# Optimization experiments

Hardware: AMD Instinct MI355X
Metric: run time of the kernel (lower is better)

Reference implementation:

```python
import jax, jax.numpy as jnp
from jax import lax
import numpy as np

B = 8192      # device_size (world_size = 1 -> batch_size == device_size)
D = 512       # projection dim
K = 2048      # number of sampled negatives per anchor
TEMP = 0.5    # temperature
EPS = 1e-8    # torch CosineSimilarity eps


def setup_inputs() -> dict:
    key = jax.random.key(0)
    k1, k2, k3 = jax.random.split(key, 3)
    z_i = jax.random.normal(k1, (B, D), dtype=jnp.float32)
    z_j = jax.random.normal(k2, (B, D), dtype=jnp.float32)
    # neg_perm = torch.randperm(batch_size - 1)[:K]
    neg_perm = jax.random.permutation(k3, B - 1)[:K].astype(jnp.int32)
    return {"z_i": z_i, "z_j": z_j, "neg_perm": neg_perm}


def _logits(z_i, z_j, neg_perm):
    # cosine similarity matrix: (zi . zj) / max(||zi||*||zj||, eps), scaled by 1/T
    ni = jnp.linalg.norm(z_i, axis=1)                       # [B]
    nj = jnp.linalg.norm(z_j, axis=1)                       # [B]
    dots = jnp.einsum('id,jd->ij', z_i, z_j)                # [B,B]
    sim = dots / jnp.maximum(ni[:, None] * nj[None, :], EPS) / TEMP

    pos = jnp.diagonal(sim)                                 # [B] positives
    # row i of sim with diagonal removed has column k -> original column k + (k>=i)
    rows = jnp.arange(B, dtype=neg_perm.dtype)[:, None]     # [B,1]
    cols = neg_perm[None, :] + (neg_perm[None, :] >= rows).astype(neg_perm.dtype)  # [B,K]
    negs = jnp.take_along_axis(sim, cols, axis=1)           # [B,K]
    logits = jnp.concatenate([pos[:, None], negs], axis=1)  # [B,1+K], label = 0
    return logits, pos


def reference(z_i, z_j, neg_perm):
    logits, pos = _logits(z_i, z_j, neg_perm)
    # log(exp(pos) + sum exp(negs)) - pos == logsumexp(logits) - pos
    loss = jnp.sum(jax.nn.logsumexp(logits, axis=1) - pos) / B
    # top-1 / top-5 accuracy against label 0
    _, pred = lax.top_k(logits, 5)                          # [B,5]
    acc1 = jnp.mean((pred[:, 0] == 0).astype(jnp.float32)) * 100.0
    acc5 = jnp.mean(jnp.any(pred == 0, axis=1).astype(jnp.float32)) * 100.0
    return loss, acc1, acc5
```

## Files before the change

### kernel.cpp

```cpp
#include <hip/hip_runtime.h>
#include <cstdint>

#define B_SZ 8192
#define D_SZ 512
#define K_SZ 2048
#define EPSV 1e-8f
#define INV_T 2.0f

typedef float floatx16 __attribute__((ext_vector_type(16)));
typedef int intx8 __attribute__((ext_vector_type(8)));

__device__ __forceinline__ void async_cp16(const void* g, void* l) {
    typedef __attribute__((address_space(1))) unsigned int gds_t;
    typedef __attribute__((address_space(3))) unsigned int lds_t;
    __builtin_amdgcn_global_load_lds((gds_t*)(unsigned long long)g, (lds_t*)l, 16, 0, 0);
}

__device__ __forceinline__ int2 pack_fp8x8(float4 a0, float4 a1) {
    int w0 = __builtin_amdgcn_cvt_pk_fp8_f32(a0.x, a0.y, 0, false);
    w0 = __builtin_amdgcn_cvt_pk_fp8_f32(a0.z, a0.w, w0, true);
    int w1 = __builtin_amdgcn_cvt_pk_fp8_f32(a1.x, a1.y, 0, false);
    w1 = __builtin_amdgcn_cvt_pk_fp8_f32(a1.z, a1.w, w1, true);
    return make_int2(w0, w1);
}

__global__ __launch_bounds__(256) void k_prep(
    const float* __restrict__ zi, const float* __restrict__ zj,
    const int* __restrict__ perm,
    float* __restrict__ ri_arr, float* __restrict__ pos_arr,
    unsigned char* __restrict__ A,
    float4* __restrict__ kmeta, unsigned char* __restrict__ G,
    float* __restrict__ rowacc, float* __restrict__ out)
{
    int w = threadIdx.x >> 6, l = threadIdx.x & 63;
    if (blockIdx.x < 2048) {
        if (blockIdx.x < 64)
            rowacc[blockIdx.x * 256 + threadIdx.x] = 0.f;
        if (blockIdx.x == 0 && threadIdx.x < 3) out[threadIdx.x] = 0.f;
        int row = blockIdx.x * 4 + w;
        const float4* zi4 = (const float4*)(zi + (size_t)row * D_SZ);
        const float4* zj4 = (const float4*)(zj + (size_t)row * D_SZ);
        float4 a0 = zi4[2 * l], a1 = zi4[2 * l + 1];
        float4 b0 = zj4[2 * l], b1 = zj4[2 * l + 1];
        float si = a0.x * a0.x + a0.y * a0.y + a0.z * a0.z + a0.w * a0.w
                 + a1.x * a1.x + a1.y * a1.y + a1.z * a1.z + a1.w * a1.w;
        float sj = b0.x * b0.x + b0.y * b0.y + b0.z * b0.z + b0.w * b0.w
                 + b1.x * b1.x + b1.y * b1.y + b1.z * b1.z + b1.w * b1.w;
        float dd = a0.x * b0.x + a0.y * b0.y + a0.z * b0.z + a0.w * b0.w
                 + a1.x * b1.x + a1.y * b1.y + a1.z * b1.z + a1.w * b1.w;
        for (int m = 1; m < 64; m <<= 1) {
            si += __shfl_xor(si, m);
            sj += __shfl_xor(sj, m);
            dd += __shfl_xor(dd, m);
        }
        if (l == 0) {
            float ni = sqrtf(si), nj = sqrtf(sj);
            ri_arr[row] = INV_T / fmaxf(ni, 1e-6f);
            pos_arr[row] = dd / fmaxf(ni * nj, EPSV) * INV_T;
        }
        *(int2*)(A + (size_t)row * D_SZ + l * 8) = pack_fp8x8(a0, a1);
    } else {
        __shared__ float srj[4];
        int g = (blockIdx.x - 2048) * 4 + w;
        int c0 = perm[g >> 1];
        int c = c0 + (g & 1);
        const float4* src = (const float4*)(zj + (size_t)c * D_SZ);
        float4 a0 = src[2 * l], a1 = src[2 * l + 1];
        float s = a0.x * a0.x + a0.y * a0.y + a0.z * a0.z + a0.w * a0.w
                + a1.x * a1.x + a1.y * a1.y + a1.z * a1.z + a1.w * a1.w;
        for (int m = 1; m < 64; m <<= 1) s += __shfl_xor(s, m);
        if (l == 0) srj[w] = 1.0f / fmaxf(sqrtf(s), 1e-6f);
        __syncthreads();
        if ((w & 1) == 0 && l == 0)
            kmeta[g >> 1] = make_float4(srj[w], srj[w + 1],
                                        __int_as_float(c0), 0.f);
        *(int2*)(G + (size_t)g * D_SZ + l * 8) = pack_fp8x8(a0, a1);
    }
}

__global__ __launch_bounds__(256, 4) void k_gemm(
    const unsigned char* __restrict__ A,
    const unsigned char* __restrict__ G,
    const float4* __restrict__ kmeta,
    const float* __restrict__ ri_arr,
    const float* __restrict__ pos_arr,
    float* __restrict__ rowacc)
{
    __shared__ unsigned char Asl[2][128 * 64];
    __shared__ unsigned char Gsl[2][128 * 64];
    const int tid = threadIdx.x;
    const int l = tid & 63, w = tid >> 6;
    const int wm = w >> 1, wn = w & 1;
    const int ln = l & 31, q = l >> 5;

    const int bid = blockIdx.x;
    const int xcd = bid & 7;
    const int slot = bid >> 3;
    const int gTile = xcd * 4 + (slot & 3);
    const int aTile = slot >> 2;
    const int gBase = gTile * 128;
    const int aBase = aTile * 128;

    size_t aOff[2], gOff[2];
    int ldsOff[2];
    #pragma unroll
    for (int it = 0; it < 2; ++it) {
        int fc = it * 256 + tid;
        int r = fc >> 2, s = fc & 3;
        int scc = s ^ ((r ^ (r >> 2)) & 3);
        aOff[it] = (size_t)(aBase + r) * D_SZ + scc * 16;
        gOff[it] = (size_t)(gBase + r) * D_SZ + scc * 16;
        ldsOff[it] = fc * 16;
    }

    floatx16 acc[2][2] = {};

    int aAddr[2][2], gAddr[2][2];
    #pragma unroll
    for (int t = 0; t < 2; ++t) {
        int ar = wn * 64 + t * 32 + ln;
        int xa = (ar ^ (ar >> 2)) & 3;
        aAddr[t][0] = ar * 64 + ((2 * q) ^ xa) * 16;
        aAddr[t][1] = ar * 64 + ((2 * q + 1) ^ xa) * 16;
        int gr = wm * 64 + t * 32 + ln;
        int xg = (gr ^ (gr >> 2)) & 3;
        gAddr[t][0] = gr * 64 + ((2 * q) ^ xg) * 16;
        gAddr[t][1] = gr * 64 + ((2 * q + 1) ^ xg) * 16;
    }

    #pragma unroll
    for (int it = 0; it < 2; ++it) {
        async_cp16(A + aOff[it], &Asl[0][ldsOff[it]]);
        async_cp16(G + gOff[it], &Gsl[0][ldsOff[it]]);
    }

    #pragma unroll 1
    for (int dblk = 0; dblk < 8; ++dblk) {
        const int cur = dblk & 1, nxt = cur ^ 1;
        __syncthreads();
        if (dblk < 7) {
            #pragma unroll
            for (int it = 0; it < 2; ++it) {
                async_cp16(A + aOff[it] + (size_t)(dblk + 1) * 64, &Asl[nxt][ldsOff[it]]);
                async_cp16(G + gOff[it] + (size_t)(dblk + 1) * 64, &Gsl[nxt][ldsOff[it]]);
            }
        }
        intx8 af[2], gf[2];
        #pragma unroll
        for (int t = 0; t < 2; ++t) {
            int4 lo = *(const int4*)&Asl[cur][aAddr[t][0]];
            int4 hi = *(const int4*)&Asl[cur][aAddr[t][1]];
            af[t][0] = lo.x; af[t][1] = lo.y; af[t][2] = lo.z; af[t][3] = lo.w;
            af[t][4] = hi.x; af[t][5] = hi.y; af[t][6] = hi.z; af[t][7] = hi.w;
            int4 glo = *(const int4*)&Gsl[cur][gAddr[t][0]];
            int4 ghi = *(const int4*)&Gsl[cur][gAddr[t][1]];
            gf[t][0] = glo.x; gf[t][1] = glo.y; gf[t][2] = glo.z; gf[t][3] = glo.w;
            gf[t][4] = ghi.x; gf[t][5] = ghi.y; gf[t][6] = ghi.z; gf[t][7] = ghi.w;
        }
        #pragma unroll
        for (int tm = 0; tm < 2; ++tm)
            #pragma unroll
            for (int tn = 0; tn < 2; ++tn)
                acc[tm][tn] = __builtin_amdgcn_mfma_scale_f32_32x32x64_f8f6f4(
                    gf[tm], af[tn], acc[tm][tn],
                    0, 0,
                    0, 0x7f7f7f7f,
                    0, 0x7f7f7f7f);
    }

    int anc[2]; float riv[2], pv[2], pe[2] = {0.f, 0.f}, pc[2] = {0.f, 0.f};
    #pragma unroll
    for (int tn = 0; tn < 2; ++tn) {
        anc[tn] = aBase + wn * 64 + tn * 32 + ln;
        riv[tn] = ri_arr[anc[tn]];
        pv[tn] = pos_arr[anc[tn]];
    }
    #pragma unroll
    for (int tm = 0; tm < 2; ++tm) {
        #pragma unroll
        for (int j = 0; j < 4; ++j) {
            int k0 = gTile * 64 + wm * 32 + tm * 16 + 4 * j + 2 * q;
            float4 m0 = kmeta[k0];
            float4 m1 = kmeta[k0 + 1];
            #pragma unroll
            for (int p = 0; p < 2; ++p) {
                float4 md = p ? m1 : m0;
                int c0 = __float_as_int(md.z);
                int re = 4 * j + 2 * p;
                #pragma unroll
                for (int tn = 0; tn < 2; ++tn) {
                    bool sel = (c0 >= anc[tn]);
                    float v = sel ? acc[tm][tn][re + 1] : acc[tm][tn][re];
                    float rj = sel ? md.y : md.x;
                    float logit = v * riv[tn] * rj;
                    pe[tn] += __expf(logit);
                    pc[tn] += (logit > pv[tn]) ? 1.f : 0.f;
                }
            }
        }
    }
    #pragma unroll
    for (int tn = 0; tn < 2; ++tn) {
        pe[tn] += __shfl_xor(pe[tn], 32);
        pc[tn] += __shfl_xor(pc[tn], 32);
        if (q == 0) {
            atomicAdd(&rowacc[anc[tn]], pe[tn]);
            atomicAdd(&rowacc[B_SZ + anc[tn]], pc[tn]);
        }
    }
}

__global__ __launch_bounds__(256) void k_final(
    const float* __restrict__ rowacc, const float* __restrict__ pos_arr,
    float* __restrict__ out)
{
    int row = blockIdx.x * 256 + threadIdx.x;
    float pe = rowacc[row];
    float pc = rowacc[B_SZ + row];
    float pos = pos_arr[row];
    float loss = logf(__expf(pos) + pe) - pos;
    float a1 = (pc < 0.5f) ? 1.f : 0.f;
    float a5 = (pc < 4.5f) ? 1.f : 0.f;
    for (int m = 1; m < 64; m <<= 1) {
        loss += __shfl_xor(loss, m);
        a1 += __shfl_xor(a1, m);
        a5 += __shfl_xor(a5, m);
    }
    __shared__ float red[3][4];
    int w = threadIdx.x >> 6, l = threadIdx.x & 63;
    if (l == 0) { red[0][w] = loss; red[1][w] = a1; red[2][w] = a5; }
    __syncthreads();
    if (threadIdx.x == 0) {
        float L = red[0][0] + red[0][1] + red[0][2] + red[0][3];
        float A1 = red[1][0] + red[1][1] + red[1][2] + red[1][3];
        float A5 = red[2][0] + red[2][1] + red[2][2] + red[2][3];
        atomicAdd(&out[0], L / (float)B_SZ);
        atomicAdd(&out[1], A1 * (100.f / (float)B_SZ));
        atomicAdd(&out[2], A5 * (100.f / (float)B_SZ));
    }
}

extern "C" void kernel_launch(void* const* d_in, const int* in_sizes, int n_in,
                              void* d_out, int out_size, void* d_ws, size_t ws_size,
                              hipStream_t stream)
{
    const float* zi = (const float*)d_in[0];
    const float* zj = (const float*)d_in[1];
    const int* perm = (const int*)d_in[2];
    float* out = (float*)d_out;

    char* p = (char*)d_ws;
    unsigned char* A = (unsigned char*)p;    p += (size_t)B_SZ * D_SZ;
    unsigned char* G = (unsigned char*)p;    p += (size_t)2 * K_SZ * D_SZ;
    float* ri_arr = (float*)p;               p += (size_t)B_SZ * 4;
    float* pos_arr = (float*)p;              p += (size_t)B_SZ * 4;
    float4* kmeta = (float4*)p;              p += (size_t)K_SZ * 16;
    float* rowacc = (float*)p;               p += (size_t)2 * B_SZ * 4;

    k_prep<<<2048 + 1024, 256, 0, stream>>>(zi, zj, perm, ri_arr, pos_arr, A,
                                            kmeta, G, rowacc, out);
    k_gemm<<<2048, 256, 0, stream>>>(A, G, kmeta, ri_arr, pos_arr, rowacc);
    k_final<<<32, 256, 0, stream>>>(rowacc, pos_arr, out);
}
```

Measured before the change: 47.44 us.

## Enlarge GEMM tiles to 256x256 with 512 threads and 4-stage async pipeline

The FP8 MFMA GEMM moves from 128x128 tiles with 4 waves to 256x256 tiles with 8 waves per block, and launches 512 blocks instead of 2048. Global-to-LDS copies become a 4-deep ring buffer with explicit vmcnt waits and raw s_barrier, plus setprio around the MFMA cluster. The aim is more data reuse per loaded byte and better overlap of loads with compute. In exchange it uses 128KB of LDS per block, which lowers occupancy. It also relies on hand-counted vmcnt values being correct.

```diff
diff --git a/kernel.cpp b/kernel.cpp
--- a/kernel.cpp
+++ b/kernel.cpp
@@ -78,7 +78,7 @@
     }
 }
 
-__global__ __launch_bounds__(256, 4) void k_gemm(
+__global__ __launch_bounds__(512, 2) void k_gemm(
     const unsigned char* __restrict__ A,
     const unsigned char* __restrict__ G,
     const float4* __restrict__ kmeta,
@@ -86,8 +86,7 @@
     const float* __restrict__ pos_arr,
     float* __restrict__ rowacc)
 {
-    __shared__ unsigned char Asl[2][128 * 64];
-    __shared__ unsigned char Gsl[2][128 * 64];
+    __shared__ unsigned char lds[4][2][16384];
     const int tid = threadIdx.x;
     const int l = tid & 63, w = tid >> 6;
     const int wm = w >> 1, wn = w & 1;
@@ -96,16 +95,16 @@
     const int bid = blockIdx.x;
     const int xcd = bid & 7;
     const int slot = bid >> 3;
-    const int gTile = xcd * 4 + (slot & 3);
-    const int aTile = slot >> 2;
-    const int gBase = gTile * 128;
-    const int aBase = aTile * 128;
+    const int gTile = xcd * 2 + (slot & 1);
+    const int aTile = slot >> 1;
+    const int gBase = gTile * 256;
+    const int aBase = aTile * 256;
 
     size_t aOff[2], gOff[2];
     int ldsOff[2];
     #pragma unroll
     for (int it = 0; it < 2; ++it) {
-        int fc = it * 256 + tid;
+        int fc = it * 512 + tid;
         int r = fc >> 2, s = fc & 3;
         int scc = s ^ ((r ^ (r >> 2)) & 3);
         aOff[it] = (size_t)(aBase + r) * D_SZ + scc * 16;
@@ -113,65 +112,80 @@
         ldsOff[it] = fc * 16;
     }
 
-    floatx16 acc[2][2] = {};
-
-    int aAddr[2][2], gAddr[2][2];
-    #pragma unroll
-    for (int t = 0; t < 2; ++t) {
-        int ar = wn * 64 + t * 32 + ln;
+#define STAGE(t_) do {                                                      \
+        unsigned char* Ad_ = &lds[(t_) & 3][0][0];                          \
+        unsigned char* Gd_ = &lds[(t_) & 3][1][0];                          \
+        size_t ko_ = (size_t)(t_) * 64;                                     \
+        async_cp16(A + aOff[0] + ko_, Ad_ + ldsOff[0]);                     \
+        async_cp16(A + aOff[1] + ko_, Ad_ + ldsOff[1]);                     \
+        async_cp16(G + gOff[0] + ko_, Gd_ + ldsOff[0]);                     \
+        async_cp16(G + gOff[1] + ko_, Gd_ + ldsOff[1]);                     \
+    } while (0)
+
+    int aAddr[4][2], gAddr[2][2];
+    #pragma unroll
+    for (int tn = 0; tn < 4; ++tn) {
+        int ar = wn * 128 + tn * 32 + ln;
         int xa = (ar ^ (ar >> 2)) & 3;
-        aAddr[t][0] = ar * 64 + ((2 * q) ^ xa) * 16;
-        aAddr[t][1] = ar * 64 + ((2 * q + 1) ^ xa) * 16;
-        int gr = wm * 64 + t * 32 + ln;
+        aAddr[tn][0] = ar * 64 + ((2 * q) ^ xa) * 16;
+        aAddr[tn][1] = ar * 64 + ((2 * q + 1) ^ xa) * 16;
+    }
+    #pragma unroll
+    for (int tm = 0; tm < 2; ++tm) {
+        int gr = wm * 64 + tm * 32 + ln;
         int xg = (gr ^ (gr >> 2)) & 3;
-        gAddr[t][0] = gr * 64 + ((2 * q) ^ xg) * 16;
-        gAddr[t][1] = gr * 64 + ((2 * q + 1) ^ xg) * 16;
-    }
-
-    #pragma unroll
-    for (int it = 0; it < 2; ++it) {
-        async_cp16(A + aOff[it], &Asl[0][ldsOff[it]]);
-        async_cp16(G + gOff[it], &Gsl[0][ldsOff[it]]);
-    }
+        gAddr[tm][0] = gr * 64 + ((2 * q) ^ xg) * 16;
+        gAddr[tm][1] = gr * 64 + ((2 * q + 1) ^ xg) * 16;
+    }
+
+    floatx16 acc[2][4] = {};
+
+    STAGE(0); STAGE(1); STAGE(2);
 
     #pragma unroll 1
-    for (int dblk = 0; dblk < 8; ++dblk) {
-        const int cur = dblk & 1, nxt = cur ^ 1;
-        __syncthreads();
-        if (dblk < 7) {
-            #pragma unroll
-            for (int it = 0; it < 2; ++it) {
-                async_cp16(A + aOff[it] + (size_t)(dblk + 1) * 64, &Asl[nxt][ldsOff[it]]);
-                async_cp16(G + gOff[it] + (size_t)(dblk + 1) * 64, &Gsl[nxt][ldsOff[it]]);
-            }
-        }
-        intx8 af[2], gf[2];
-        #pragma unroll
-        for (int t = 0; t < 2; ++t) {
-            int4 lo = *(const int4*)&Asl[cur][aAddr[t][0]];
-            int4 hi = *(const int4*)&Asl[cur][aAddr[t][1]];
-            af[t][0] = lo.x; af[t][1] = lo.y; af[t][2] = lo.z; af[t][3] = lo.w;
-            af[t][4] = hi.x; af[t][5] = hi.y; af[t][6] = hi.z; af[t][7] = hi.w;
-            int4 glo = *(const int4*)&Gsl[cur][gAddr[t][0]];
-            int4 ghi = *(const int4*)&Gsl[cur][gAddr[t][1]];
-            gf[t][0] = glo.x; gf[t][1] = glo.y; gf[t][2] = glo.z; gf[t][3] = glo.w;
-            gf[t][4] = ghi.x; gf[t][5] = ghi.y; gf[t][6] = ghi.z; gf[t][7] = ghi.w;
-        }
+    for (int t = 0; t < 8; ++t) {
+        if (t < 6)       asm volatile("s_waitcnt vmcnt(8)" ::: "memory");
+        else if (t == 6) asm volatile("s_waitcnt vmcnt(4)" ::: "memory");
+        else             asm volatile("s_waitcnt vmcnt(0)" ::: "memory");
+        __builtin_amdgcn_s_barrier();
+        __builtin_amdgcn_sched_barrier(0);
+        if (t < 5) STAGE(t + 3);
+        const unsigned char* Ab = &lds[t & 3][0][0];
+        const unsigned char* Gb = &lds[t & 3][1][0];
+        intx8 af[4], gf[2];
+        #pragma unroll
+        for (int tn = 0; tn < 4; ++tn) {
+            int4 lo = *(const int4*)(Ab + aAddr[tn][0]);
+            int4 hi = *(const int4*)(Ab + aAddr[tn][1]);
+            af[tn][0] = lo.x; af[tn][1] = lo.y; af[tn][2] = lo.z; af[tn][3] = lo.w;
+            af[tn][4] = hi.x; af[tn][5] = hi.y; af[tn][6] = hi.z; af[tn][7] = hi.w;
+        }
+        #pragma unroll
+        for (int tm = 0; tm < 2; ++tm) {
+            int4 lo = *(const int4*)(Gb + gAddr[tm][0]);
+            int4 hi = *(const int4*)(Gb + gAddr[tm][1]);
+            gf[tm][0] = lo.x; gf[tm][1] = lo.y; gf[tm][2] = lo.z; gf[tm][3] = lo.w;
+            gf[tm][4] = hi.x; gf[tm][5] = hi.y; gf[tm][6] = hi.z; gf[tm][7] = hi.w;
+        }
+        __builtin_amdgcn_s_setprio(1);
         #pragma unroll
         for (int tm = 0; tm < 2; ++tm)
             #pragma unroll
-            for (int tn = 0; tn < 2; ++tn)
+            for (int tn = 0; tn < 4; ++tn)
                 acc[tm][tn] = __builtin_amdgcn_mfma_scale_f32_32x32x64_f8f6f4(
                     gf[tm], af[tn], acc[tm][tn],
                     0, 0,
                     0, 0x7f7f7f7f,
                     0, 0x7f7f7f7f);
-    }
-
-    int anc[2]; float riv[2], pv[2], pe[2] = {0.f, 0.f}, pc[2] = {0.f, 0.f};
-    #pragma unroll
-    for (int tn = 0; tn < 2; ++tn) {
-        anc[tn] = aBase + wn * 64 + tn * 32 + ln;
+        __builtin_amdgcn_s_setprio(0);
+    }
+#undef STAGE
+
+    int anc[4]; float riv[4], pv[4];
+    float pe[4] = {0.f, 0.f, 0.f, 0.f}, pc[4] = {0.f, 0.f, 0.f, 0.f};
+    #pragma unroll
+    for (int tn = 0; tn < 4; ++tn) {
+        anc[tn] = aBase + wn * 128 + tn * 32 + ln;
         riv[tn] = ri_arr[anc[tn]];
         pv[tn] = pos_arr[anc[tn]];
     }
@@ -179,7 +193,7 @@
     for (int tm = 0; tm < 2; ++tm) {
         #pragma unroll
         for (int j = 0; j < 4; ++j) {
-            int k0 = gTile * 64 + wm * 32 + tm * 16 + 4 * j + 2 * q;
+            int k0 = gTile * 128 + wm * 32 + tm * 16 + 4 * j + 2 * q;
             float4 m0 = kmeta[k0];
             float4 m1 = kmeta[k0 + 1];
             #pragma unroll
@@ -188,7 +202,7 @@
                 int c0 = __float_as_int(md.z);
                 int re = 4 * j + 2 * p;
                 #pragma unroll
-                for (int tn = 0; tn < 2; ++tn) {
+                for (int tn = 0; tn < 4; ++tn) {
                     bool sel = (c0 >= anc[tn]);
                     float v = sel ? acc[tm][tn][re + 1] : acc[tm][tn][re];
                     float rj = sel ? md.y : md.x;
@@ -200,7 +214,7 @@
         }
     }
     #pragma unroll
-    for (int tn = 0; tn < 2; ++tn) {
+    for (int tn = 0; tn < 4; ++tn) {
         pe[tn] += __shfl_xor(pe[tn], 32);
         pc[tn] += __shfl_xor(pc[tn], 32);
         if (q == 0) {
@@ -259,6 +273,6 @@
 
     k_prep<<<2048 + 1024, 256, 0, stream>>>(zi, zj, perm, ri_arr, pos_arr, A,
                                             kmeta, G, rowacc, out);
-    k_gemm<<<2048, 256, 0, stream>>>(A, G, kmeta, ri_arr, pos_arr, rowacc);
+    k_gemm<<<512, 512, 0, stream>>>(A, G, kmeta, ri_arr, pos_arr, rowacc);
     k_final<<<32, 256, 0, stream>>>(rowacc, pos_arr, out);
 }
```

Result: slower. 52.07 us (+9.8%).

## Sort negatives by column and split into shifted/unshifted halves to skip tiles

Applied to the files above, without the earlier changes.

The prep kernel now ranks each sampled negative by its column index, a counting sort done with a full pass over the permutation in every block. It writes the unshifted (c0) and shifted (c0+1) rows of z_j into two separate sorted halves of G, each with its own metadata. Each GEMM block handles one half and exits early when the tile's column range cannot contribute to its anchor rows (v=0 needs c0 < anchor, v=1 needs c0 >= anchor). This drops roughly half of the MFMA work in exchange for an O(K) rank computation per prep block and uneven block lifetimes.

```diff
diff --git a/kernel.cpp b/kernel.cpp
--- a/kernel.cpp
+++ b/kernel.cpp
@@ -29,7 +29,7 @@
     const int* __restrict__ perm,
     float* __restrict__ ri_arr, float* __restrict__ pos_arr,
     unsigned char* __restrict__ A,
-    float4* __restrict__ kmeta, unsigned char* __restrict__ G,
+    float2* __restrict__ meta, unsigned char* __restrict__ G,
     float* __restrict__ rowacc, float* __restrict__ out)
 {
     int w = threadIdx.x >> 6, l = threadIdx.x & 63;
@@ -60,32 +60,69 @@
         }
         *(int2*)(A + (size_t)row * D_SZ + l * 8) = pack_fp8x8(a0, a1);
     } else {
-        __shared__ float srj[4];
-        int g = (blockIdx.x - 2048) * 4 + w;
-        int c0 = perm[g >> 1];
-        int c = c0 + (g & 1);
+        __shared__ int rpart[2][4];
+        int bg = blockIdx.x - 2048;
+        int k0 = bg * 2;
+        int c0a = perm[k0], c0b = perm[k0 + 1];
+        int cnta = 0, cntb = 0;
+        for (int j = threadIdx.x; j < K_SZ; j += 256) {
+            int p = perm[j];
+            cnta += (p < c0a) ? 1 : 0;
+            cntb += (p < c0b) ? 1 : 0;
+        }
+        for (int m = 1; m < 64; m <<= 1) {
+            cnta += __shfl_xor(cnta, m);
+            cntb += __shfl_xor(cntb, m);
+        }
+        if (l == 0) { rpart[0][w] = cnta; rpart[1][w] = cntb; }
+        __syncthreads();
+        int ra = rpart[0][0] + rpart[0][1] + rpart[0][2] + rpart[0][3];
+        int rb = rpart[1][0] + rpart[1][1] + rpart[1][2] + rpart[1][3];
+        int myc0   = (w >> 1) ? c0b : c0a;
+        int myrank = (w >> 1) ? rb : ra;
+        int vv = w & 1;
+        int c = myc0 + vv;
         const float4* src = (const float4*)(zj + (size_t)c * D_SZ);
         float4 a0 = src[2 * l], a1 = src[2 * l + 1];
         float s = a0.x * a0.x + a0.y * a0.y + a0.z * a0.z + a0.w * a0.w
                 + a1.x * a1.x + a1.y * a1.y + a1.z * a1.z + a1.w * a1.w;
         for (int m = 1; m < 64; m <<= 1) s += __shfl_xor(s, m);
-        if (l == 0) srj[w] = 1.0f / fmaxf(sqrtf(s), 1e-6f);
-        __syncthreads();
-        if ((w & 1) == 0 && l == 0)
-            kmeta[g >> 1] = make_float4(srj[w], srj[w + 1],
-                                        __int_as_float(c0), 0.f);
-        *(int2*)(G + (size_t)g * D_SZ + l * 8) = pack_fp8x8(a0, a1);
+        if (l == 0) {
+            float rj = 1.0f / fmaxf(sqrtf(s), 1e-6f);
+            meta[vv * K_SZ + myrank] = make_float2(rj, __int_as_float(myc0));
+        }
+        *(int2*)(G + ((size_t)(vv * K_SZ + myrank)) * D_SZ + l * 8) =
+            pack_fp8x8(a0, a1);
     }
 }
 
 __global__ __launch_bounds__(256, 4) void k_gemm(
     const unsigned char* __restrict__ A,
     const unsigned char* __restrict__ G,
-    const float4* __restrict__ kmeta,
+    const float2* __restrict__ meta,
     const float* __restrict__ ri_arr,
     const float* __restrict__ pos_arr,
     float* __restrict__ rowacc)
 {
+    const int bid = blockIdx.x;
+    const int xcd = bid & 7;
+    const int rest = bid >> 3;
+    const int v = rest & 1;
+    const int slot = rest >> 1;
+    const int gTile = xcd * 2 + (slot & 1);
+    const int aTile = slot >> 1;
+    const int gBase = gTile * 128;
+    const int aBase = aTile * 128;
+    const float2* mv = meta + v * K_SZ;
+
+    if (v == 0) {
+        int c0min = __float_as_int(mv[gBase].y);
+        if (c0min >= aBase + 127) return;
+    } else {
+        int c0max = __float_as_int(mv[gBase + 127].y);
+        if (c0max < aBase) return;
+    }
+
     __shared__ unsigned char Asl[2][128 * 64];
     __shared__ unsigned char Gsl[2][128 * 64];
     const int tid = threadIdx.x;
@@ -93,14 +130,6 @@
     const int wm = w >> 1, wn = w & 1;
     const int ln = l & 31, q = l >> 5;
 
-    const int bid = blockIdx.x;
-    const int xcd = bid & 7;
-    const int slot = bid >> 3;
-    const int gTile = xcd * 4 + (slot & 3);
-    const int aTile = slot >> 2;
-    const int gBase = gTile * 128;
-    const int aBase = aTile * 128;
-
     size_t aOff[2], gOff[2];
     int ldsOff[2];
     #pragma unroll
@@ -109,7 +138,7 @@
         int r = fc >> 2, s = fc & 3;
         int scc = s ^ ((r ^ (r >> 2)) & 3);
         aOff[it] = (size_t)(aBase + r) * D_SZ + scc * 16;
-        gOff[it] = (size_t)(gBase + r) * D_SZ + scc * 16;
+        gOff[it] = (size_t)(v * K_SZ + gBase + r) * D_SZ + scc * 16;
         ldsOff[it] = fc * 16;
     }
 
@@ -179,22 +208,19 @@
     for (int tm = 0; tm < 2; ++tm) {
         #pragma unroll
         for (int j = 0; j < 4; ++j) {
-            int k0 = gTile * 64 + wm * 32 + tm * 16 + 4 * j + 2 * q;
-            float4 m0 = kmeta[k0];
-            float4 m1 = kmeta[k0 + 1];
             #pragma unroll
-            for (int p = 0; p < 2; ++p) {
-                float4 md = p ? m1 : m0;
-                int c0 = __float_as_int(md.z);
-                int re = 4 * j + 2 * p;
+            for (int b = 0; b < 4; ++b) {
+                int re = 4 * j + b;
+                int k = gBase + wm * 64 + tm * 32 + 4 * q + b + 8 * j;
+                float2 md = mv[k];
+                float rj = md.x;
+                int c0 = __float_as_int(md.y);
                 #pragma unroll
                 for (int tn = 0; tn < 2; ++tn) {
-                    bool sel = (c0 >= anc[tn]);
-                    float v = sel ? acc[tm][tn][re + 1] : acc[tm][tn][re];
-                    float rj = sel ? md.y : md.x;
-                    float logit = v * riv[tn] * rj;
-                    pe[tn] += __expf(logit);
-                    pc[tn] += (logit > pv[tn]) ? 1.f : 0.f;
+                    bool inc = v ? (c0 >= anc[tn]) : (c0 < anc[tn]);
+                    float logit = acc[tm][tn][re] * riv[tn] * rj;
+                    pe[tn] += inc ? __expf(logit) : 0.f;
+                    pc[tn] += (inc && logit > pv[tn]) ? 1.f : 0.f;
                 }
             }
         }
@@ -254,11 +280,11 @@
     unsigned char* G = (unsigned char*)p;    p += (size_t)2 * K_SZ * D_SZ;
     float* ri_arr = (float*)p;               p += (size_t)B_SZ * 4;
     float* pos_arr = (float*)p;              p += (size_t)B_SZ * 4;
-    float4* kmeta = (float4*)p;              p += (size_t)K_SZ * 16;
+    float2* meta = (float2*)p;               p += (size_t)2 * K_SZ * 8;
     float* rowacc = (float*)p;               p += (size_t)2 * B_SZ * 4;
 
     k_prep<<<2048 + 1024, 256, 0, stream>>>(zi, zj, perm, ri_arr, pos_arr, A,
-                                            kmeta, G, rowacc, out);
-    k_gemm<<<2048, 256, 0, stream>>>(A, G, kmeta, ri_arr, pos_arr, rowacc);
+                                            meta, G, rowacc, out);
+    k_gemm<<<2048, 256, 0, stream>>>(A, G, meta, ri_arr, pos_arr, rowacc);
     k_final<<<32, 256, 0, stream>>>(rowacc, pos_arr, out);
 }
```

New measurement: 49.83 us. 5.0% more time.

## Process two G tiles per block with a single continuous pipelined K loop

Applied to the files above, without the earlier changes.

Each GEMM block now handles a pair of 128-row G tiles in sequence instead of one, halving the grid to 1024 blocks. The double-buffered async load loop runs across both tiles, so the prefetch for the second tile overlaps the first tile's epilogue, and the A-row metadata is loaded once. The aim is to cut per-block launch and prologue/epilogue overhead and keep the pipeline full. In exchange the grid has less parallelism, and since A tiles are reloaded per G tile there is no extra reuse.

```diff
diff --git a/kernel.cpp b/kernel.cpp
--- a/kernel.cpp
+++ b/kernel.cpp
@@ -96,12 +96,11 @@
     const int bid = blockIdx.x;
     const int xcd = bid & 7;
     const int slot = bid >> 3;
-    const int gTile = xcd * 4 + (slot & 3);
-    const int aTile = slot >> 2;
-    const int gBase = gTile * 128;
+    const int gPair = xcd * 2 + (slot & 1);
+    const int aTile = slot >> 1;
     const int aBase = aTile * 128;
 
-    size_t aOff[2], gOff[2];
+    size_t aOff[2], gOff0[2];
     int ldsOff[2];
     #pragma unroll
     for (int it = 0; it < 2; ++it) {
@@ -109,9 +108,10 @@
         int r = fc >> 2, s = fc & 3;
         int scc = s ^ ((r ^ (r >> 2)) & 3);
         aOff[it] = (size_t)(aBase + r) * D_SZ + scc * 16;
-        gOff[it] = (size_t)(gBase + r) * D_SZ + scc * 16;
+        gOff0[it] = (size_t)(gPair * 256 + r) * D_SZ + scc * 16;
         ldsOff[it] = fc * 16;
     }
+    const size_t gHalfStride = (size_t)128 * D_SZ;
 
     floatx16 acc[2][2] = {};
 
@@ -128,21 +128,32 @@
         gAddr[t][1] = gr * 64 + ((2 * q + 1) ^ xg) * 16;
     }
 
+    int anc[2]; float riv[2], pv[2];
+    #pragma unroll
+    for (int tn = 0; tn < 2; ++tn) {
+        anc[tn] = aBase + wn * 64 + tn * 32 + ln;
+        riv[tn] = ri_arr[anc[tn]];
+        pv[tn] = pos_arr[anc[tn]];
+    }
+
     #pragma unroll
     for (int it = 0; it < 2; ++it) {
         async_cp16(A + aOff[it], &Asl[0][ldsOff[it]]);
-        async_cp16(G + gOff[it], &Gsl[0][ldsOff[it]]);
+        async_cp16(G + gOff0[it], &Gsl[0][ldsOff[it]]);
     }
 
     #pragma unroll 1
-    for (int dblk = 0; dblk < 8; ++dblk) {
-        const int cur = dblk & 1, nxt = cur ^ 1;
+    for (int s = 0; s < 16; ++s) {
+        const int cur = s & 1, nxt = cur ^ 1;
         __syncthreads();
-        if (dblk < 7) {
+        if (s < 15) {
+            const int s1 = s + 1;
+            const size_t kO = (size_t)(s1 & 7) * 64;
+            const size_t gH = (s1 >> 3) ? gHalfStride : 0;
             #pragma unroll
             for (int it = 0; it < 2; ++it) {
-                async_cp16(A + aOff[it] + (size_t)(dblk + 1) * 64, &Asl[nxt][ldsOff[it]]);
-                async_cp16(G + gOff[it] + (size_t)(dblk + 1) * 64, &Gsl[nxt][ldsOff[it]]);
+                async_cp16(A + aOff[it] + kO, &Asl[nxt][ldsOff[it]]);
+                async_cp16(G + gOff0[it] + gH + kO, &Gsl[nxt][ldsOff[it]]);
             }
         }
         intx8 af[2], gf[2];
@@ -166,46 +177,50 @@
                     0, 0,
                     0, 0x7f7f7f7f,
                     0, 0x7f7f7f7f);
-    }
-
-    int anc[2]; float riv[2], pv[2], pe[2] = {0.f, 0.f}, pc[2] = {0.f, 0.f};
-    #pragma unroll
-    for (int tn = 0; tn < 2; ++tn) {
-        anc[tn] = aBase + wn * 64 + tn * 32 + ln;
-        riv[tn] = ri_arr[anc[tn]];
-        pv[tn] = pos_arr[anc[tn]];
-    }
-    #pragma unroll
-    for (int tm = 0; tm < 2; ++tm) {
-        #pragma unroll
-        for (int j = 0; j < 4; ++j) {
-            int k0 = gTile * 64 + wm * 32 + tm * 16 + 4 * j + 2 * q;
-            float4 m0 = kmeta[k0];
-            float4 m1 = kmeta[k0 + 1];
-            #pragma unroll
-            for (int p = 0; p < 2; ++p) {
-                float4 md = p ? m1 : m0;
-                int c0 = __float_as_int(md.z);
-                int re = 4 * j + 2 * p;
+
+        if ((s & 7) == 7) {
+            const int gT = gPair * 2 + (s >> 3);
+            float pe[2] = {0.f, 0.f}, pc[2] = {0.f, 0.f};
+            #pragma unroll
+            for (int tm = 0; tm < 2; ++tm) {
                 #pragma unroll
-                for (int tn = 0; tn < 2; ++tn) {
-                    bool sel = (c0 >= anc[tn]);
-                    float v = sel ? acc[tm][tn][re + 1] : acc[tm][tn][re];
-                    float rj = sel ? md.y : md.x;
-                    float logit = v * riv[tn] * rj;
-                    pe[tn] += __expf(logit);
-                    pc[tn] += (logit > pv[tn]) ? 1.f : 0.f;
+                for (int j = 0; j < 4; ++j) {
+                    int k0 = gT * 64 + wm * 32 + tm * 16 + 4 * j + 2 * q;
+                    float4 m0 = kmeta[k0];
+                    float4 m1 = kmeta[k0 + 1];
+                    #pragma unroll
+                    for (int p = 0; p < 2; ++p) {
+                        float4 md = p ? m1 : m0;
+                        int c0 = __float_as_int(md.z);
+                        int re = 4 * j + 2 * p;
+                        #pragma unroll
+                        for (int tn = 0; tn < 2; ++tn) {
+                            bool sel = (c0 >= anc[tn]);
+                            float v = sel ? acc[tm][tn][re + 1] : acc[tm][tn][re];
+                            float rj = sel ? md.y : md.x;
+                            float logit = v * riv[tn] * rj;
+                            pe[tn] += __expf(logit);
+                            pc[tn] += (logit > pv[tn]) ? 1.f : 0.f;
+                        }
+                    }
                 }
             }
-        }
-    }
-    #pragma unroll
-    for (int tn = 0; tn < 2; ++tn) {
-        pe[tn] += __shfl_xor(pe[tn], 32);
-        pc[tn] += __shfl_xor(pc[tn], 32);
-        if (q == 0) {
-            atomicAdd(&rowacc[anc[tn]], pe[tn]);
-            atomicAdd(&rowacc[B_SZ + anc[tn]], pc[tn]);
+            #pragma unroll
+            for (int tn = 0; tn < 2; ++tn) {
+                pe[tn] += __shfl_xor(pe[tn], 32);
+                pc[tn] += __shfl_xor(pc[tn], 32);
+                if (q == 0) {
+                    atomicAdd(&rowacc[anc[tn]], pe[tn]);
+                    atomicAdd(&rowacc[B_SZ + anc[tn]], pc[tn]);
+                }
+            }
+            #pragma unroll
+            for (int tm = 0; tm < 2; ++tm)
+                #pragma unroll
+                for (int tn = 0; tn < 2; ++tn)
+                    #pragma unroll
+                    for (int e = 0; e < 16; ++e)
+                        acc[tm][tn][e] = 0.f;
         }
     }
 }
@@ -259,6 +274,6 @@
 
     k_prep<<<2048 + 1024, 256, 0, stream>>>(zi, zj, perm, ri_arr, pos_arr, A,
                                             kmeta, G, rowacc, out);
-    k_gemm<<<2048, 256, 0, stream>>>(A, G, kmeta, ri_arr, pos_arr, rowacc);
+    k_gemm<<<1024, 256, 0, stream>>>(A, G, kmeta, ri_arr, pos_arr, rowacc);
     k_final<<<32, 256, 0, stream>>>(rowacc, pos_arr, out);
 }
```

Result: slower. 64.02 us (+35.0%).
